# Kernel tuning notes

Measured on AMD Instinct MI355X. Metric: run time of the kernel, lower is better.

## Reference

```python
import jax, jax.numpy as jnp
import numpy as np

ADMP = 16  # admp_channel


def _backbone(x, Wc, bc):
    # Conv2d(3->256, k=3, stride=2, pad=1) + ReLU stands in for feature_backbone
    y = jax.lax.conv_general_dilated(x, Wc, window_strides=(2, 2),
                                     padding=((1, 1), (1, 1)),
                                     dimension_numbers=('NCHW', 'OIHW', 'NCHW'))
    return jax.nn.relu(y + bc[None, :, None, None])


def _feature_select(feat, k):
    # AdaptiveMaxPool2d(k, return_indices=True) on feat.sum(1); H,W divisible by k
    B, C, H, W = feat.shape
    bh, bw = H // k, W // k
    resp = feat.sum(1)  # [B,H,W]
    r = resp.reshape(B, k, bh, k, bw).transpose(0, 1, 3, 2, 4).reshape(B, k, k, bh * bw)
    loc = jnp.argmax(r, axis=-1)            # local flat index in each bh*bw block
    lr, lc = loc // bw, loc % bw
    rows = jnp.arange(k)[None, :, None] * bh + lr   # [B,k,k]
    cols = jnp.arange(k)[None, None, :] * bw + lc
    return (rows * W + cols).reshape(B, k * k)      # flat indices into H*W


def _mlp(x, W1, b1, W2, b2):
    # Linear -> ReLU -> (Dropout eval = identity) -> Linear
    return jax.nn.relu(x @ W1 + b1) @ W2 + b2


def reference(xA, xB, Wconv, bconv, W1r, b1r, W2r, b2r, W1c, b1c, W2c, b2c):
    fA = _backbone(xA, Wconv, bconv)  # [B,C,H,W]
    fB = _backbone(xB, Wconv, bconv)
    B, C, H, W = fA.shape
    N = H * W
    idxA = _feature_select(fA, ADMP)                       # [B,K]
    fA_flat = fA.reshape(B, C, N)
    fB_flat = fB.reshape(B, C, N)
    desc = jnp.take_along_axis(fA_flat, idxA[:, None, :], axis=2)  # [B,C,K]
    # ||a-b||^2 = ||a||^2 - 2 a.b + ||b||^2 ; fused batched kNN
    dist = ((desc ** 2).sum(1)[:, :, None]
            - 2.0 * jnp.einsum('bck,bcn->bkn', desc, fB_flat)
            + (fB_flat ** 2).sum(1)[:, None, :])           # [B,K,N]
    minidx = jnp.argmin(dist, axis=-1)                     # [B,K]
    # original uses high (==width here since H==W) for both div and mod
    row_A, col_A = idxA // H, idxA % H
    row_B, col_B = minidx // H, minidx % H
    drow = (row_B - row_A).astype(jnp.float32)             # [B,K]
    dcol = (col_A - col_B).astype(jnp.float32)
    out_drow = _mlp(drow, W1r, b1r, W2r, b2r)              # [B,1]
    out_dcol = _mlp(dcol, W1c, b1c, W2c, b2c)
    return jnp.concatenate([out_drow, out_dcol], axis=1)   # [B,2]


def setup_inputs() -> dict:
    key = jax.random.key(0)
    ks = jax.random.split(key, 8)
    K2 = ADMP * ADMP
    return {
        'xA': jax.random.normal(ks[0], (4, 3, 256, 256), jnp.float32),
        'xB': jax.random.normal(ks[1], (4, 3, 256, 256), jnp.float32),
        'Wconv': jax.random.normal(ks[2], (256, 3, 3, 3), jnp.float32) * 0.1,
        'bconv': jnp.zeros((256,), jnp.float32),
        'W1r': jax.random.normal(ks[3], (K2, K2 // 2), jnp.float32) * 0.05,
        'b1r': jnp.zeros((K2 // 2,), jnp.float32),
        'W2r': jax.random.normal(ks[4], (K2 // 2, 1), jnp.float32) * 0.05,
        'b2r': jnp.zeros((1,), jnp.float32),
        'W1c': jax.random.normal(ks[5], (K2, K2 // 2), jnp.float32) * 0.05,
        'b1c': jnp.zeros((K2 // 2,), jnp.float32),
        'W2c': jax.random.normal(ks[6], (K2 // 2, 1), jnp.float32) * 0.05,
        'b2c': jnp.zeros((1,), jnp.float32),
    }
```

## Files before the change

### kernel.cpp

```cpp
#include <hip/hip_runtime.h>
#include <stdint.h>

constexpr int NB   = 4;
constexpr int CIN  = 3;
constexpr int HIN  = 256;
constexpr int COUT = 256;
constexpr int HF   = 128;
constexpr int NF   = HF * HF;
constexpr int KADM = 16;
constexpr int KK   = KADM * KADM;
constexpr int HID  = 128;
constexpr int DFB  = 65536;
constexpr int PX   = 32;
constexpr int NT   = NF / PX;

typedef unsigned short ushort_t;
typedef __attribute__((ext_vector_type(8))) _Float16 f16x8;
typedef __attribute__((ext_vector_type(2))) __fp16   fp16v2;
typedef __attribute__((ext_vector_type(4))) float    f32x4;

__device__ inline unsigned long long u64min(unsigned long long a, unsigned long long b) {
    return a < b ? a : b;
}
__device__ inline ushort_t f16bits(_Float16 h) { return __builtin_bit_cast(ushort_t, h); }

__device__ inline int swz(int pix, int c) {
    return pix * 256 + ((((c >> 3) ^ (pix & 7)) << 3) | (c & 7));
}

__device__ inline int dfoff(int w, int chunk, int j, int lane) {
    return (((w * 8 + chunk) * 4 + j) * 64 + lane) * 8;
}

__global__ __launch_bounds__(256) void prep_kernel(
        const float* __restrict__ W, ushort_t* __restrict__ WFh, ushort_t* __restrict__ WFl)
{
    int co = threadIdx.x;
    int w = co >> 6, j = (co >> 4) & 3, la = co & 15;
    #pragma unroll
    for (int q = 0; q < 32; ++q) {
        float v = (q < 27) ? W[co * 27 + q] : 0.f;
        _Float16 h = (_Float16)v;
        _Float16 l = (_Float16)(v - (float)h);
        int lg = q >> 3, e = q & 7;
        int off = ((w * 4 + j) * 64 + lg * 16 + la) * 8 + e;
        WFh[off] = f16bits(h);
        WFl[off] = f16bits(l);
    }
}

__global__ __launch_bounds__(256) void convA_kernel(
        const float* __restrict__ xA,
        const ushort_t* __restrict__ WFh, const ushort_t* __restrict__ WFl,
        const float* __restrict__ bias, float* __restrict__ resp)
{
    __shared__ float    pS[CIN][3][132];
    __shared__ ushort_t Ah[64][40];
    __shared__ ushort_t Al[64][40];
    __shared__ float    redS[4][64];

    int b = blockIdx.y;
    const float* x = xA + (size_t)b * CIN * HIN * HIN;
    int tid = threadIdx.x;
    int lane = tid & 63, w = tid >> 6;
    int la = lane & 15, lg = lane >> 4;
    int wbase = w * 64;

    float bj[4];
    f16x8 bh[4], bl[4];
    #pragma unroll
    for (int j = 0; j < 4; ++j) {
        bj[j] = bias[wbase + j * 16 + la];
        int off = ((w * 4 + j) * 64 + lane) * 8;
        bh[j] = *(const f16x8*)&WFh[off];
        bl[j] = *(const f16x8*)&WFl[off];
    }

    for (int t2 = 0; t2 < 2; ++t2) {
        int tile = blockIdx.x * 2 + t2;
        int oh  = tile >> 1;
        int ow0 = (tile & 1) << 6;

        if (t2) __syncthreads();
        for (int i = tid; i < CIN * 3 * 129; i += 256) {
            int ci = i / (3 * 129);
            int r2 = i % (3 * 129);
            int kh = r2 / 129, c = r2 % 129;
            int gr = 2 * oh - 1 + kh, gc = 2 * ow0 - 1 + c;
            float v = 0.f;
            if (gr >= 0 && gr < HIN && gc >= 0 && gc < HIN)
                v = x[(size_t)ci * HIN * HIN + (size_t)gr * HIN + gc];
            pS[ci][kh][c] = v;
        }
        __syncthreads();

        {
            int n = tid >> 2, qg = tid & 3;
            unsigned uh[4], ul[4];
            #pragma unroll
            for (int e2 = 0; e2 < 4; ++e2) {
                ushort_t hh[2], ll[2];
                #pragma unroll
                for (int s = 0; s < 2; ++s) {
                    int q = qg * 8 + e2 * 2 + s;
                    float v = 0.f;
                    if (q < 27) {
                        int ci = q / 9, r = (q % 9) / 3, kw = q % 3;
                        v = pS[ci][r][2 * n + kw];
                    }
                    _Float16 h = (_Float16)v;
                    _Float16 l = (_Float16)(v - (float)h);
                    hh[s] = f16bits(h); ll[s] = f16bits(l);
                }
                uh[e2] = (unsigned)hh[0] | ((unsigned)hh[1] << 16);
                ul[e2] = (unsigned)ll[0] | ((unsigned)ll[1] << 16);
            }
            *(uint4*)&Ah[n][qg * 8] = *(uint4*)uh;
            *(uint4*)&Al[n][qg * 8] = *(uint4*)ul;
        }
        __syncthreads();

        f16x8 ah[4], al[4];
        #pragma unroll
        for (int i = 0; i < 4; ++i) {
            ah[i] = *(const f16x8*)&Ah[i * 16 + la][lg * 8];
            al[i] = *(const f16x8*)&Al[i * 16 + la][lg * 8];
        }

        f32x4 acc[4][4];
        #pragma unroll
        for (int i = 0; i < 4; ++i)
            #pragma unroll
            for (int j = 0; j < 4; ++j) acc[i][j] = (f32x4)0.f;

        #pragma unroll
        for (int i = 0; i < 4; ++i)
            #pragma unroll
            for (int j = 0; j < 4; ++j) {
                acc[i][j] = __builtin_amdgcn_mfma_f32_16x16x32_f16(ah[i], bh[j], acc[i][j], 0, 0, 0);
                acc[i][j] = __builtin_amdgcn_mfma_f32_16x16x32_f16(al[i], bh[j], acc[i][j], 0, 0, 0);
                acc[i][j] = __builtin_amdgcn_mfma_f32_16x16x32_f16(ah[i], bl[j], acc[i][j], 0, 0, 0);
            }

        float s[4][4];
        #pragma unroll
        for (int i = 0; i < 4; ++i)
            #pragma unroll
            for (int r = 0; r < 4; ++r) s[i][r] = 0.f;

        #pragma unroll
        for (int i = 0; i < 4; ++i)
            #pragma unroll
            for (int j = 0; j < 4; ++j)
                #pragma unroll
                for (int r = 0; r < 4; ++r)
                    s[i][r] += fmaxf(acc[i][j][r] + bj[j], 0.f);

        #pragma unroll
        for (int i = 0; i < 4; ++i)
            #pragma unroll
            for (int r = 0; r < 4; ++r) {
                float v = s[i][r];
                v += __shfl_xor(v, 1, 64);
                v += __shfl_xor(v, 2, 64);
                v += __shfl_xor(v, 4, 64);
                v += __shfl_xor(v, 8, 64);
                s[i][r] = v;
            }
        if (la == 0) {
            #pragma unroll
            for (int i = 0; i < 4; ++i)
                #pragma unroll
                for (int r = 0; r < 4; ++r)
                    redS[w][i * 16 + lg * 4 + r] = s[i][r];
        }
        __syncthreads();
        if (tid < 64) {
            float tot = redS[0][tid] + redS[1][tid] + redS[2][tid] + redS[3][tid];
            resp[(size_t)b * NF + oh * HF + ow0 + tid] = tot;
        }
    }
}

__global__ __launch_bounds__(256) void select_kernel(
        const float* __restrict__ resp,
        const float* __restrict__ xA, const float* __restrict__ W,
        const float* __restrict__ bias,
        int* __restrict__ idxA,
        ushort_t* __restrict__ dFh, ushort_t* __restrict__ dFl,
        float* __restrict__ normA)
{
    __shared__ float patch[27];
    __shared__ float red[4];
    __shared__ int   sidx;

    int bk = blockIdx.x;
    int b = bk >> 8, k = bk & 255;
    int t = threadIdx.x;

    if (t < 64) {
        int kr = k >> 4, kc = k & 15;
        int lr = t >> 3, lc = t & 7;
        int row = kr * 8 + lr, col = kc * 8 + lc;
        float bv = resp[(size_t)b * NF + (size_t)row * HF + col];
        int best = t;
        for (int off = 32; off > 0; off >>= 1) {
            float ov = __shfl_down(bv, off, 64);
            int   oi = __shfl_down(best, off, 64);
            if (ov > bv || (ov == bv && oi < best)) { bv = ov; best = oi; }
        }
        if (t == 0) {
            int r = kr * 8 + (best >> 3), c = kc * 8 + (best & 7);
            int idx = r * HF + c;
            idxA[bk] = idx;
            sidx = idx;
        }
    }
    __syncthreads();
    int idx = sidx;
    int oh = idx >> 7, ow = idx & 127;

    if (t < 27) {
        int ci = t / 9, kh = (t % 9) / 3, kw = t % 3;
        int ir = oh * 2 - 1 + kh, ic = ow * 2 - 1 + kw;
        float v = 0.f;
        if (ir >= 0 && ir < HIN && ic >= 0 && ic < HIN)
            v = xA[((size_t)b * CIN + ci) * HIN * HIN + (size_t)ir * HIN + ic];
        patch[t] = v;
    }
    __syncthreads();

    float v = bias[t];
    const float* w = &W[t * 27];
    #pragma unroll
    for (int q = 0; q < 27; ++q) v = fmaf(patch[q], w[q], v);
    v = fmaxf(v, 0.f);

    _Float16 h = (_Float16)v;
    _Float16 l = (_Float16)(v - (float)h);
    {
        int wq = k >> 6, j = (k >> 4) & 3, la = k & 15;
        int chunk = t >> 5, lg = (t >> 3) & 3, e = t & 7;
        int off = b * DFB + dfoff(wq, chunk, j, lg * 16 + la) + e;
        dFh[off] = f16bits(h);
        dFl[off] = f16bits(l);
    }

    float s = v * v;
    for (int off = 32; off > 0; off >>= 1) s += __shfl_down(s, off, 64);
    if ((t & 63) == 0) red[t >> 6] = s;
    __syncthreads();
    if (t == 0) normA[bk] = red[0] + red[1] + red[2] + red[3];
}

__device__ inline void load_desc(const ushort_t* __restrict__ dFh,
                                 const ushort_t* __restrict__ dFl,
                                 int w, int chunk, int lane,
                                 f16x8* bh, f16x8* bl)
{
    #pragma unroll
    for (int j = 0; j < 4; ++j) {
        int off = dfoff(w, chunk, j, lane);
        bh[j] = *(const f16x8*)&dFh[off];
        bl[j] = *(const f16x8*)&dFl[off];
    }
}

__device__ inline void knn_chunk(const ushort_t* __restrict__ fH,
                                 const ushort_t* __restrict__ fL,
                                 int la, int lg, int cc,
                                 const f16x8* bh, const f16x8* bl,
                                 f32x4 (&acc)[2][4])
{
    #pragma unroll
    for (int i = 0; i < 2; ++i) {
        f16x8 ah = *(const f16x8*)&fH[swz(i * 16 + la, cc + lg * 8)];
        f16x8 al = *(const f16x8*)&fL[swz(i * 16 + la, cc + lg * 8)];
        __builtin_amdgcn_s_setprio(1);
        #pragma unroll
        for (int j = 0; j < 4; ++j) {
            acc[i][j] = __builtin_amdgcn_mfma_f32_16x16x32_f16(ah, bh[j], acc[i][j], 0, 0, 0);
            acc[i][j] = __builtin_amdgcn_mfma_f32_16x16x32_f16(al, bh[j], acc[i][j], 0, 0, 0);
            acc[i][j] = __builtin_amdgcn_mfma_f32_16x16x32_f16(ah, bl[j], acc[i][j], 0, 0, 0);
        }
        __builtin_amdgcn_s_setprio(0);
    }
}

__global__ __launch_bounds__(256, 4) void fused_kernel(
        const float* __restrict__ xB,
        const ushort_t* __restrict__ WFh, const ushort_t* __restrict__ WFl,
        const float* __restrict__ bias,
        const ushort_t* __restrict__ dFhg, const ushort_t* __restrict__ dFlg,
        const float* __restrict__ normA,
        unsigned long long* __restrict__ packed)
{
    __shared__ __align__(16) char smem[2 * PX * 256 * 2];
    __shared__ float redS[4][PX];
    __shared__ float nAS[KK];
    __shared__ float nBS[PX];
    __shared__ float bS[COUT];

    float*    pSp = (float*)smem;
    ushort_t* AhP = (ushort_t*)(smem + 2448);
    ushort_t* AlP = (ushort_t*)(smem + 2448 + 2560);
    ushort_t* fH  = (ushort_t*)smem;
    ushort_t* fL  = (ushort_t*)(smem + PX * 256 * 2);

    int tile = blockIdx.x;
    int b    = blockIdx.y;
    int oh   = tile >> 2;
    int ow0  = (tile & 3) << 5;
    const float* x = xB + (size_t)b * CIN * HIN * HIN;
    int tid = threadIdx.x;

    nAS[tid] = normA[b * KK + tid];
    bS[tid]  = bias[tid];

    for (int i = tid; i < CIN * 3 * 65; i += 256) {
        int ci = i / (3 * 65);
        int r2 = i % (3 * 65);
        int kh = r2 / 65, c = r2 % 65;
        int gr = 2 * oh - 1 + kh, gc = 2 * ow0 - 1 + c;
        float v = 0.f;
        if (gr >= 0 && gr < HIN && gc >= 0 && gc < HIN)
            v = x[(size_t)ci * HIN * HIN + (size_t)gr * HIN + gc];
        pSp[ci * 204 + kh * 68 + c] = v;
    }
    __syncthreads();

    {
        int n = tid >> 3, qg = tid & 7;
        ushort_t hh[4], ll[4];
        #pragma unroll
        for (int s = 0; s < 4; ++s) {
            int q = qg * 4 + s;
            float v = 0.f;
            if (q < 27) {
                int ci = q / 9, r = (q % 9) / 3, kw = q % 3;
                v = pSp[ci * 204 + r * 68 + 2 * n + kw];
            }
            _Float16 h = (_Float16)v;
            _Float16 l = (_Float16)(v - (float)h);
            hh[s] = f16bits(h); ll[s] = f16bits(l);
        }
        unsigned lo, hi;
        lo = (unsigned)hh[0] | ((unsigned)hh[1] << 16);
        hi = (unsigned)hh[2] | ((unsigned)hh[3] << 16);
        *(uint2*)&AhP[n * 40 + qg * 4] = make_uint2(lo, hi);
        lo = (unsigned)ll[0] | ((unsigned)ll[1] << 16);
        hi = (unsigned)ll[2] | ((unsigned)ll[3] << 16);
        *(uint2*)&AlP[n * 40 + qg * 4] = make_uint2(lo, hi);
    }
    __syncthreads();

    int lane = tid & 63, w = tid >> 6;
    int la = lane & 15, lg = lane >> 4;
    int wbase = w * 64;

    f16x8 wah[4], wal[4], pbh[2], pbl[2];
    #pragma unroll
    for (int j = 0; j < 4; ++j) {
        int off = ((w * 4 + j) * 64 + lane) * 8;
        wah[j] = *(const f16x8*)&WFh[off];
        wal[j] = *(const f16x8*)&WFl[off];
    }
    #pragma unroll
    for (int i = 0; i < 2; ++i) {
        pbh[i] = *(const f16x8*)&AhP[(i * 16 + la) * 40 + lg * 8];
        pbl[i] = *(const f16x8*)&AlP[(i * 16 + la) * 40 + lg * 8];
    }

    f32x4 cacc[4][2];
    #pragma unroll
    for (int j = 0; j < 4; ++j)
        #pragma unroll
        for (int i = 0; i < 2; ++i) cacc[j][i] = (f32x4)0.f;

    #pragma unroll
    for (int j = 0; j < 4; ++j)
        #pragma unroll
        for (int i = 0; i < 2; ++i) {
            cacc[j][i] = __builtin_amdgcn_mfma_f32_16x16x32_f16(wah[j], pbh[i], cacc[j][i], 0, 0, 0);
            cacc[j][i] = __builtin_amdgcn_mfma_f32_16x16x32_f16(wal[j], pbh[i], cacc[j][i], 0, 0, 0);
            cacc[j][i] = __builtin_amdgcn_mfma_f32_16x16x32_f16(wah[j], pbl[i], cacc[j][i], 0, 0, 0);
        }

    __syncthreads();

    float s2[2] = {0.f, 0.f};
    #pragma unroll
    for (int j = 0; j < 4; ++j) {
        f32x4 b4 = *(const f32x4*)&bS[wbase + j * 16 + lg * 4];
        int chunk = (wbase + j * 16 + lg * 4) >> 3;
        int within = (lg & 1) * 4;
        #pragma unroll
        for (int i = 0; i < 2; ++i) {
            int pix = i * 16 + la;
            float v0 = fmaxf(cacc[j][i][0] + b4[0], 0.f);
            float v1 = fmaxf(cacc[j][i][1] + b4[1], 0.f);
            float v2 = fmaxf(cacc[j][i][2] + b4[2], 0.f);
            float v3 = fmaxf(cacc[j][i][3] + b4[3], 0.f);
            s2[i] += v0 * v0 + v1 * v1 + v2 * v2 + v3 * v3;
            fp16v2 h01 = __builtin_amdgcn_cvt_pkrtz(v0, v1);
            fp16v2 h23 = __builtin_amdgcn_cvt_pkrtz(v2, v3);
            fp16v2 l01 = __builtin_amdgcn_cvt_pkrtz(v0 - (float)h01[0], v1 - (float)h01[1]);
            fp16v2 l23 = __builtin_amdgcn_cvt_pkrtz(v2 - (float)h23[0], v3 - (float)h23[1]);
            int base = pix * 256 + ((chunk ^ (pix & 7)) << 3) + within;
            *(uint2*)&fH[base] = make_uint2(__builtin_bit_cast(unsigned, h01),
                                            __builtin_bit_cast(unsigned, h23));
            *(uint2*)&fL[base] = make_uint2(__builtin_bit_cast(unsigned, l01),
                                            __builtin_bit_cast(unsigned, l23));
        }
    }

    const ushort_t* dFh = dFhg + (size_t)b * DFB;
    const ushort_t* dFl = dFlg + (size_t)b * DFB;
    f16x8 bhA[4], blA[4], bhB[4], blB[4];
    load_desc(dFh, dFl, w, 0, lane, bhA, blA);
    load_desc(dFh, dFl, w, 1, lane, bhB, blB);

    #pragma unroll
    for (int i = 0; i < 2; ++i) {
        float v = s2[i];
        v += __shfl_xor(v, 16, 64);
        v += __shfl_xor(v, 32, 64);
        if (lg == 0) redS[w][i * 16 + la] = v;
    }
    __syncthreads();
    if (tid < PX) nBS[tid] = redS[0][tid] + redS[1][tid] + redS[2][tid] + redS[3][tid];
    __syncthreads();

    f32x4 acc[2][4];
    #pragma unroll
    for (int i = 0; i < 2; ++i)
        #pragma unroll
        for (int j = 0; j < 4; ++j) acc[i][j] = (f32x4)0.f;

    knn_chunk(fH, fL, la, lg, 0, bhA, blA, acc);
    load_desc(dFh, dFl, w, 2, lane, bhA, blA);
    knn_chunk(fH, fL, la, lg, 32, bhB, blB, acc);
    load_desc(dFh, dFl, w, 3, lane, bhB, blB);
    knn_chunk(fH, fL, la, lg, 64, bhA, blA, acc);
    load_desc(dFh, dFl, w, 4, lane, bhA, blA);
    knn_chunk(fH, fL, la, lg, 96, bhB, blB, acc);
    load_desc(dFh, dFl, w, 5, lane, bhB, blB);
    knn_chunk(fH, fL, la, lg, 128, bhA, blA, acc);
    load_desc(dFh, dFl, w, 6, lane, bhA, blA);
    knn_chunk(fH, fL, la, lg, 160, bhB, blB, acc);
    load_desc(dFh, dFl, w, 7, lane, bhB, blB);
    knn_chunk(fH, fL, la, lg, 192, bhA, blA, acc);
    knn_chunk(fH, fL, la, lg, 224, bhB, blB, acc);

    float nBv[2][4];
    #pragma unroll
    for (int i = 0; i < 2; ++i) {
        f32x4 t4 = *(const f32x4*)&nBS[i * 16 + lg * 4];
        nBv[i][0] = t4[0]; nBv[i][1] = t4[1]; nBv[i][2] = t4[2]; nBv[i][3] = t4[3];
    }
    int n0 = tile * PX;
    float bd[4];
    int   bn[4];
    #pragma unroll
    for (int j = 0; j < 4; ++j) {
        int kl = wbase + j * 16 + la;
        float nAv = nAS[kl];
        float bestd = 3.4e38f;
        int   bestn = 0;
        #pragma unroll
        for (int i = 0; i < 2; ++i)
            #pragma unroll
            for (int r = 0; r < 4; ++r) {
                int n = n0 + i * 16 + lg * 4 + r;
                float d = fmaf(-2.f, acc[i][j][r], nAv) + nBv[i][r];
                if (d < bestd) { bestd = d; bestn = n; }
            }
        #pragma unroll
        for (int off = 16; off <= 32; off <<= 1) {
            float od = __shfl_xor(bestd, off, 64);
            int   on = __shfl_xor(bestn, off, 64);
            bool take = (od < bestd) || (od == bestd && on < bestn);
            bestd = take ? od : bestd;
            bestn = take ? on : bestn;
        }
        bd[j] = bestd; bn[j] = bestn;
    }
    float fd = (lg == 0) ? bd[0] : (lg == 1) ? bd[1] : (lg == 2) ? bd[2] : bd[3];
    int   fn = (lg == 0) ? bn[0] : (lg == 1) ? bn[1] : (lg == 2) ? bn[2] : bn[3];
    unsigned u = __float_as_uint(fd);
    u = (u & 0x80000000u) ? ~u : (u | 0x80000000u);
    unsigned long long key = ((unsigned long long)u << 32) | (unsigned)fn;
    int klw = wbase + lg * 16 + la;
    atomicMin(&packed[b * KK + klw], key);
}

__global__ __launch_bounds__(128) void mlp_kernel(
        const int* __restrict__ idxA, const unsigned long long* __restrict__ packed,
        const float* __restrict__ W1r, const float* __restrict__ b1r,
        const float* __restrict__ W2r, const float* __restrict__ b2r,
        const float* __restrict__ W1c, const float* __restrict__ b1c,
        const float* __restrict__ W2c, const float* __restrict__ b2c,
        float* __restrict__ out)
{
    __shared__ float xS[KK];
    __shared__ float red[2];
    int blk = blockIdx.x;
    int b = blk >> 1, which = blk & 1;
    int t = threadIdx.x;

    for (int k = t; k < KK; k += 128) {
        int ia = idxA[b * KK + k];
        int nn = (int)(packed[b * KK + k] & 0xffffffffULL);
        int rowA = ia >> 7, colA = ia & 127;
        int rowB = nn >> 7, colB = nn & 127;
        xS[k] = (which == 0) ? (float)(rowB - rowA) : (float)(colA - colB);
    }
    __syncthreads();

    const float* W1 = which ? W1c : W1r;
    const float* b1 = which ? b1c : b1r;
    const float* W2 = which ? W2c : W2r;
    const float* b2 = which ? b2c : b2r;

    float h = b1[t];
    for (int k = 0; k < KK; ++k) h = fmaf(xS[k], W1[k * HID + t], h);
    h = fmaxf(h, 0.f);
    float pv = h * W2[t];
    for (int off = 32; off > 0; off >>= 1) pv += __shfl_down(pv, off, 64);
    if ((t & 63) == 0) red[t >> 6] = pv;
    __syncthreads();
    if (t == 0) out[b * 2 + which] = red[0] + red[1] + b2[0];
}

extern "C" void kernel_launch(void* const* d_in, const int* in_sizes, int n_in,
                              void* d_out, int out_size, void* d_ws, size_t ws_size,
                              hipStream_t stream)
{
    const float* xA  = (const float*)d_in[0];
    const float* xB  = (const float*)d_in[1];
    const float* Wc  = (const float*)d_in[2];
    const float* bc  = (const float*)d_in[3];
    const float* W1r = (const float*)d_in[4];
    const float* b1r = (const float*)d_in[5];
    const float* W2r = (const float*)d_in[6];
    const float* b2r = (const float*)d_in[7];
    const float* W1c = (const float*)d_in[8];
    const float* b1c = (const float*)d_in[9];
    const float* W2c = (const float*)d_in[10];
    const float* b2c = (const float*)d_in[11];
    float* out = (float*)d_out;

    char* ws = (char*)d_ws;
    unsigned long long* packed = (unsigned long long*)ws; ws += (size_t)NB * KK * 8;
    int*   idxA   = (int*)ws;      ws += (size_t)NB * KK * 4;
    float* normA  = (float*)ws;    ws += (size_t)NB * KK * 4;
    float* resp   = (float*)ws;    ws += (size_t)NB * NF * 4;
    ushort_t* dFh = (ushort_t*)ws; ws += (size_t)NB * DFB * 2;
    ushort_t* dFl = (ushort_t*)ws; ws += (size_t)NB * DFB * 2;
    ushort_t* WFh = (ushort_t*)ws; ws += (size_t)COUT * 32 * 2;
    ushort_t* WFl = (ushort_t*)ws; ws += (size_t)COUT * 32 * 2;

    hipMemsetAsync(packed, 0xFF, (size_t)NB * KK * 8, stream);

    prep_kernel  <<<1, 256, 0, stream>>>(Wc, WFh, WFl);
    convA_kernel <<<dim3(128, NB), 256, 0, stream>>>(xA, WFh, WFl, bc, resp);
    select_kernel<<<NB * KK, 256, 0, stream>>>(resp, xA, Wc, bc, idxA, dFh, dFl, normA);
    fused_kernel <<<dim3(NT, NB), 256, 0, stream>>>(xB, WFh, WFl, bc, dFh, dFl,
                                                    normA, packed);
    mlp_kernel   <<<8, 128, 0, stream>>>(idxA, packed,
                                         W1r, b1r, W2r, b2r,
                                         W1c, b1c, W2c, b2c, out);
}
```

Before: 72.04 us.

## Double fused kernel pixel tile to 64 with 512 threads; un-loop convA tiles

The fused conv+kNN kernel now processes 64 pixels per block with 8 waves, each wave owning 32 descriptors instead of 64. The weight and descriptor fragment layouts are reorganized per 16-wide k-tile to match, and each lane group handles 4 pixel sub-tiles. This halves the number of blocks and the per-block atomicMin traffic and descriptor reloads, and makes the staged input patch more reusable. convA drops its two-tiles-per-block loop and launches one tile per block instead. In exchange, the larger shared-memory footprint and 512-thread blocks may reduce occupancy.

```diff
diff --git a/kernel.cpp b/kernel.cpp
--- a/kernel.cpp
+++ b/kernel.cpp
@@ -11,7 +11,7 @@
 constexpr int KK   = KADM * KADM;
 constexpr int HID  = 128;
 constexpr int DFB  = 65536;
-constexpr int PX   = 32;
+constexpr int PX   = 64;
 constexpr int NT   = NF / PX;
 
 typedef unsigned short ushort_t;
@@ -19,31 +19,28 @@
 typedef __attribute__((ext_vector_type(2))) __fp16   fp16v2;
 typedef __attribute__((ext_vector_type(4))) float    f32x4;
 
-__device__ inline unsigned long long u64min(unsigned long long a, unsigned long long b) {
-    return a < b ? a : b;
-}
 __device__ inline ushort_t f16bits(_Float16 h) { return __builtin_bit_cast(ushort_t, h); }
 
 __device__ inline int swz(int pix, int c) {
     return pix * 256 + ((((c >> 3) ^ (pix & 7)) << 3) | (c & 7));
 }
 
-__device__ inline int dfoff(int w, int chunk, int j, int lane) {
-    return (((w * 8 + chunk) * 4 + j) * 64 + lane) * 8;
+__device__ inline int dfoff(int kt, int chunk, int lane) {
+    return ((kt * 8 + chunk) * 64 + lane) * 8;
 }
 
 __global__ __launch_bounds__(256) void prep_kernel(
         const float* __restrict__ W, ushort_t* __restrict__ WFh, ushort_t* __restrict__ WFl)
 {
     int co = threadIdx.x;
-    int w = co >> 6, j = (co >> 4) & 3, la = co & 15;
+    int kt = co >> 4, la = co & 15;
     #pragma unroll
     for (int q = 0; q < 32; ++q) {
         float v = (q < 27) ? W[co * 27 + q] : 0.f;
         _Float16 h = (_Float16)v;
         _Float16 l = (_Float16)(v - (float)h);
         int lg = q >> 3, e = q & 7;
-        int off = ((w * 4 + j) * 64 + lg * 16 + la) * 8 + e;
+        int off = (kt * 64 + lg * 16 + la) * 8 + e;
         WFh[off] = f16bits(h);
         WFl[off] = f16bits(l);
     }
@@ -59,9 +56,51 @@
     __shared__ ushort_t Al[64][40];
     __shared__ float    redS[4][64];
 
-    int b = blockIdx.y;
+    int tile = blockIdx.x;
+    int b    = blockIdx.y;
+    int oh   = tile >> 1;
+    int ow0  = (tile & 1) << 6;
     const float* x = xA + (size_t)b * CIN * HIN * HIN;
     int tid = threadIdx.x;
+
+    for (int i = tid; i < CIN * 3 * 129; i += 256) {
+        int ci = i / (3 * 129);
+        int r2 = i % (3 * 129);
+        int kh = r2 / 129, c = r2 % 129;
+        int gr = 2 * oh - 1 + kh, gc = 2 * ow0 - 1 + c;
+        float v = 0.f;
+        if (gr >= 0 && gr < HIN && gc >= 0 && gc < HIN)
+            v = x[(size_t)ci * HIN * HIN + (size_t)gr * HIN + gc];
+        pS[ci][kh][c] = v;
+    }
+    __syncthreads();
+
+    {
+        int n = tid >> 2, qg = tid & 3;
+        unsigned uh[4], ul[4];
+        #pragma unroll
+        for (int e2 = 0; e2 < 4; ++e2) {
+            ushort_t hh[2], ll[2];
+            #pragma unroll
+            for (int s = 0; s < 2; ++s) {
+                int q = qg * 8 + e2 * 2 + s;
+                float v = 0.f;
+                if (q < 27) {
+                    int ci = q / 9, r = (q % 9) / 3, kw = q % 3;
+                    v = pS[ci][r][2 * n + kw];
+                }
+                _Float16 h = (_Float16)v;
+                _Float16 l = (_Float16)(v - (float)h);
+                hh[s] = f16bits(h); ll[s] = f16bits(l);
+            }
+            uh[e2] = (unsigned)hh[0] | ((unsigned)hh[1] << 16);
+            ul[e2] = (unsigned)ll[0] | ((unsigned)ll[1] << 16);
+        }
+        *(uint4*)&Ah[n][qg * 8] = *(uint4*)uh;
+        *(uint4*)&Al[n][qg * 8] = *(uint4*)ul;
+    }
+    __syncthreads();
+
     int lane = tid & 63, w = tid >> 6;
     int la = lane & 15, lg = lane >> 4;
     int wbase = w * 64;
@@ -76,109 +115,64 @@
         bl[j] = *(const f16x8*)&WFl[off];
     }
 
-    for (int t2 = 0; t2 < 2; ++t2) {
-        int tile = blockIdx.x * 2 + t2;
-        int oh  = tile >> 1;
-        int ow0 = (tile & 1) << 6;
-
-        if (t2) __syncthreads();
-        for (int i = tid; i < CIN * 3 * 129; i += 256) {
-            int ci = i / (3 * 129);
-            int r2 = i % (3 * 129);
-            int kh = r2 / 129, c = r2 % 129;
-            int gr = 2 * oh - 1 + kh, gc = 2 * ow0 - 1 + c;
-            float v = 0.f;
-            if (gr >= 0 && gr < HIN && gc >= 0 && gc < HIN)
-                v = x[(size_t)ci * HIN * HIN + (size_t)gr * HIN + gc];
-            pS[ci][kh][c] = v;
-        }
-        __syncthreads();
-
-        {
-            int n = tid >> 2, qg = tid & 3;
-            unsigned uh[4], ul[4];
+    f16x8 ah[4], al[4];
+    #pragma unroll
+    for (int i = 0; i < 4; ++i) {
+        ah[i] = *(const f16x8*)&Ah[i * 16 + la][lg * 8];
+        al[i] = *(const f16x8*)&Al[i * 16 + la][lg * 8];
+    }
+
+    f32x4 acc[4][4];
+    #pragma unroll
+    for (int i = 0; i < 4; ++i)
+        #pragma unroll
+        for (int j = 0; j < 4; ++j) acc[i][j] = (f32x4)0.f;
+
+    #pragma unroll
+    for (int i = 0; i < 4; ++i)
+        #pragma unroll
+        for (int j = 0; j < 4; ++j) {
+            acc[i][j] = __builtin_amdgcn_mfma_f32_16x16x32_f16(ah[i], bh[j], acc[i][j], 0, 0, 0);
+            acc[i][j] = __builtin_amdgcn_mfma_f32_16x16x32_f16(al[i], bh[j], acc[i][j], 0, 0, 0);
+            acc[i][j] = __builtin_amdgcn_mfma_f32_16x16x32_f16(ah[i], bl[j], acc[i][j], 0, 0, 0);
+        }
+
+    float s[4][4];
+    #pragma unroll
+    for (int i = 0; i < 4; ++i)
+        #pragma unroll
+        for (int r = 0; r < 4; ++r) s[i][r] = 0.f;
+
+    #pragma unroll
+    for (int i = 0; i < 4; ++i)
+        #pragma unroll
+        for (int j = 0; j < 4; ++j)
             #pragma unroll
-            for (int e2 = 0; e2 < 4; ++e2) {
-                ushort_t hh[2], ll[2];
-                #pragma unroll
-                for (int s = 0; s < 2; ++s) {
-                    int q = qg * 8 + e2 * 2 + s;
-                    float v = 0.f;
-                    if (q < 27) {
-                        int ci = q / 9, r = (q % 9) / 3, kw = q % 3;
-                        v = pS[ci][r][2 * n + kw];
-                    }
-                    _Float16 h = (_Float16)v;
-                    _Float16 l = (_Float16)(v - (float)h);
-                    hh[s] = f16bits(h); ll[s] = f16bits(l);
-                }
-                uh[e2] = (unsigned)hh[0] | ((unsigned)hh[1] << 16);
-                ul[e2] = (unsigned)ll[0] | ((unsigned)ll[1] << 16);
-            }
-            *(uint4*)&Ah[n][qg * 8] = *(uint4*)uh;
-            *(uint4*)&Al[n][qg * 8] = *(uint4*)ul;
-        }
-        __syncthreads();
-
-        f16x8 ah[4], al[4];
-        #pragma unroll
-        for (int i = 0; i < 4; ++i) {
-            ah[i] = *(const f16x8*)&Ah[i * 16 + la][lg * 8];
-            al[i] = *(const f16x8*)&Al[i * 16 + la][lg * 8];
-        }
-
-        f32x4 acc[4][4];
+            for (int r = 0; r < 4; ++r)
+                s[i][r] += fmaxf(acc[i][j][r] + bj[j], 0.f);
+
+    #pragma unroll
+    for (int i = 0; i < 4; ++i)
+        #pragma unroll
+        for (int r = 0; r < 4; ++r) {
+            float v = s[i][r];
+            v += __shfl_xor(v, 1, 64);
+            v += __shfl_xor(v, 2, 64);
+            v += __shfl_xor(v, 4, 64);
+            v += __shfl_xor(v, 8, 64);
+            s[i][r] = v;
+        }
+    if (la == 0) {
         #pragma unroll
         for (int i = 0; i < 4; ++i)
             #pragma unroll
-            for (int j = 0; j < 4; ++j) acc[i][j] = (f32x4)0.f;
-
-        #pragma unroll
-        for (int i = 0; i < 4; ++i)
-            #pragma unroll
-            for (int j = 0; j < 4; ++j) {
-                acc[i][j] = __builtin_amdgcn_mfma_f32_16x16x32_f16(ah[i], bh[j], acc[i][j], 0, 0, 0);
-                acc[i][j] = __builtin_amdgcn_mfma_f32_16x16x32_f16(al[i], bh[j], acc[i][j], 0, 0, 0);
-                acc[i][j] = __builtin_amdgcn_mfma_f32_16x16x32_f16(ah[i], bl[j], acc[i][j], 0, 0, 0);
-            }
-
-        float s[4][4];
-        #pragma unroll
-        for (int i = 0; i < 4; ++i)
-            #pragma unroll
-            for (int r = 0; r < 4; ++r) s[i][r] = 0.f;
-
-        #pragma unroll
-        for (int i = 0; i < 4; ++i)
-            #pragma unroll
-            for (int j = 0; j < 4; ++j)
-                #pragma unroll
-                for (int r = 0; r < 4; ++r)
-                    s[i][r] += fmaxf(acc[i][j][r] + bj[j], 0.f);
-
-        #pragma unroll
-        for (int i = 0; i < 4; ++i)
-            #pragma unroll
-            for (int r = 0; r < 4; ++r) {
-                float v = s[i][r];
-                v += __shfl_xor(v, 1, 64);
-                v += __shfl_xor(v, 2, 64);
-                v += __shfl_xor(v, 4, 64);
-                v += __shfl_xor(v, 8, 64);
-                s[i][r] = v;
-            }
-        if (la == 0) {
-            #pragma unroll
-            for (int i = 0; i < 4; ++i)
-                #pragma unroll
-                for (int r = 0; r < 4; ++r)
-                    redS[w][i * 16 + lg * 4 + r] = s[i][r];
-        }
-        __syncthreads();
-        if (tid < 64) {
-            float tot = redS[0][tid] + redS[1][tid] + redS[2][tid] + redS[3][tid];
-            resp[(size_t)b * NF + oh * HF + ow0 + tid] = tot;
-        }
+            for (int r = 0; r < 4; ++r)
+                redS[w][i * 16 + lg * 4 + r] = s[i][r];
+    }
+    __syncthreads();
+    if (tid < 64) {
+        float tot = redS[0][tid] + redS[1][tid] + redS[2][tid] + redS[3][tid];
+        resp[(size_t)b * NF + oh * HF + ow0 + tid] = tot;
     }
 }
 
@@ -239,9 +233,9 @@
     _Float16 h = (_Float16)v;
     _Float16 l = (_Float16)(v - (float)h);
     {
-        int wq = k >> 6, j = (k >> 4) & 3, la = k & 15;
+        int kt = k >> 4, la = k & 15;
         int chunk = t >> 5, lg = (t >> 3) & 3, e = t & 7;
-        int off = b * DFB + dfoff(wq, chunk, j, lg * 16 + la) + e;
+        int off = b * DFB + dfoff(kt, chunk, lg * 16 + la) + e;
         dFh[off] = f16bits(h);
         dFl[off] = f16bits(l);
     }
@@ -259,10 +253,10 @@
                                  f16x8* bh, f16x8* bl)
 {
     #pragma unroll
-    for (int j = 0; j < 4; ++j) {
-        int off = dfoff(w, chunk, j, lane);
-        bh[j] = *(const f16x8*)&dFh[off];
-        bl[j] = *(const f16x8*)&dFl[off];
+    for (int jj = 0; jj < 2; ++jj) {
+        int off = dfoff(w * 2 + jj, chunk, lane);
+        bh[jj] = *(const f16x8*)&dFh[off];
+        bl[jj] = *(const f16x8*)&dFl[off];
     }
 }
 
@@ -270,24 +264,24 @@
                                  const ushort_t* __restrict__ fL,
                                  int la, int lg, int cc,
                                  const f16x8* bh, const f16x8* bl,
-                                 f32x4 (&acc)[2][4])
-{
-    #pragma unroll
-    for (int i = 0; i < 2; ++i) {
+                                 f32x4 (&acc)[4][2])
+{
+    #pragma unroll
+    for (int i = 0; i < 4; ++i) {
         f16x8 ah = *(const f16x8*)&fH[swz(i * 16 + la, cc + lg * 8)];
         f16x8 al = *(const f16x8*)&fL[swz(i * 16 + la, cc + lg * 8)];
         __builtin_amdgcn_s_setprio(1);
         #pragma unroll
-        for (int j = 0; j < 4; ++j) {
-            acc[i][j] = __builtin_amdgcn_mfma_f32_16x16x32_f16(ah, bh[j], acc[i][j], 0, 0, 0);
-            acc[i][j] = __builtin_amdgcn_mfma_f32_16x16x32_f16(al, bh[j], acc[i][j], 0, 0, 0);
-            acc[i][j] = __builtin_amdgcn_mfma_f32_16x16x32_f16(ah, bl[j], acc[i][j], 0, 0, 0);
+        for (int jj = 0; jj < 2; ++jj) {
+            acc[i][jj] = __builtin_amdgcn_mfma_f32_16x16x32_f16(ah, bh[jj], acc[i][jj], 0, 0, 0);
+            acc[i][jj] = __builtin_amdgcn_mfma_f32_16x16x32_f16(al, bh[jj], acc[i][jj], 0, 0, 0);
+            acc[i][jj] = __builtin_amdgcn_mfma_f32_16x16x32_f16(ah, bl[jj], acc[i][jj], 0, 0, 0);
         }
         __builtin_amdgcn_s_setprio(0);
     }
 }
 
-__global__ __launch_bounds__(256, 4) void fused_kernel(
+__global__ __launch_bounds__(512, 4) void fused_kernel(
         const float* __restrict__ xB,
         const ushort_t* __restrict__ WFh, const ushort_t* __restrict__ WFl,
         const float* __restrict__ bias,
@@ -296,36 +290,38 @@
         unsigned long long* __restrict__ packed)
 {
     __shared__ __align__(16) char smem[2 * PX * 256 * 2];
-    __shared__ float redS[4][PX];
+    __shared__ float redS[8][PX];
     __shared__ float nAS[KK];
     __shared__ float nBS[PX];
     __shared__ float bS[COUT];
 
     float*    pSp = (float*)smem;
-    ushort_t* AhP = (ushort_t*)(smem + 2448);
-    ushort_t* AlP = (ushort_t*)(smem + 2448 + 2560);
+    ushort_t* AhP = (ushort_t*)(smem + 4752);
+    ushort_t* AlP = (ushort_t*)(smem + 4752 + 5120);
     ushort_t* fH  = (ushort_t*)smem;
     ushort_t* fL  = (ushort_t*)(smem + PX * 256 * 2);
 
     int tile = blockIdx.x;
     int b    = blockIdx.y;
-    int oh   = tile >> 2;
-    int ow0  = (tile & 3) << 5;
+    int oh   = tile >> 1;
+    int ow0  = (tile & 1) << 6;
     const float* x = xB + (size_t)b * CIN * HIN * HIN;
     int tid = threadIdx.x;
 
-    nAS[tid] = normA[b * KK + tid];
-    bS[tid]  = bias[tid];
-
-    for (int i = tid; i < CIN * 3 * 65; i += 256) {
-        int ci = i / (3 * 65);
-        int r2 = i % (3 * 65);
-        int kh = r2 / 65, c = r2 % 65;
+    if (tid < KK) {
+        nAS[tid] = normA[b * KK + tid];
+        bS[tid]  = bias[tid];
+    }
+
+    for (int i = tid; i < CIN * 3 * 129; i += 512) {
+        int ci = i / (3 * 129);
+        int r2 = i % (3 * 129);
+        int kh = r2 / 129, c = r2 % 129;
         int gr = 2 * oh - 1 + kh, gc = 2 * ow0 - 1 + c;
         float v = 0.f;
         if (gr >= 0 && gr < HIN && gc >= 0 && gc < HIN)
             v = x[(size_t)ci * HIN * HIN + (size_t)gr * HIN + gc];
-        pSp[ci * 204 + kh * 68 + c] = v;
+        pSp[ci * 396 + kh * 132 + c] = v;
     }
     __syncthreads();
 
@@ -338,7 +334,7 @@
             float v = 0.f;
             if (q < 27) {
                 int ci = q / 9, r = (q % 9) / 3, kw = q % 3;
-                v = pSp[ci * 204 + r * 68 + 2 * n + kw];
+                v = pSp[ci * 396 + r * 132 + 2 * n + kw];
             }
             _Float16 h = (_Float16)v;
             _Float16 l = (_Float16)(v - (float)h);
@@ -356,51 +352,51 @@
 
     int lane = tid & 63, w = tid >> 6;
     int la = lane & 15, lg = lane >> 4;
-    int wbase = w * 64;
-
-    f16x8 wah[4], wal[4], pbh[2], pbl[2];
-    #pragma unroll
-    for (int j = 0; j < 4; ++j) {
-        int off = ((w * 4 + j) * 64 + lane) * 8;
-        wah[j] = *(const f16x8*)&WFh[off];
-        wal[j] = *(const f16x8*)&WFl[off];
-    }
-    #pragma unroll
-    for (int i = 0; i < 2; ++i) {
+
+    f16x8 wah[2], wal[2], pbh[4], pbl[4];
+    #pragma unroll
+    for (int jj = 0; jj < 2; ++jj) {
+        int off = ((w * 2 + jj) * 64 + lane) * 8;
+        wah[jj] = *(const f16x8*)&WFh[off];
+        wal[jj] = *(const f16x8*)&WFl[off];
+    }
+    #pragma unroll
+    for (int i = 0; i < 4; ++i) {
         pbh[i] = *(const f16x8*)&AhP[(i * 16 + la) * 40 + lg * 8];
         pbl[i] = *(const f16x8*)&AlP[(i * 16 + la) * 40 + lg * 8];
     }
 
-    f32x4 cacc[4][2];
-    #pragma unroll
-    for (int j = 0; j < 4; ++j)
-        #pragma unroll
-        for (int i = 0; i < 2; ++i) cacc[j][i] = (f32x4)0.f;
-
-    #pragma unroll
-    for (int j = 0; j < 4; ++j)
-        #pragma unroll
-        for (int i = 0; i < 2; ++i) {
-            cacc[j][i] = __builtin_amdgcn_mfma_f32_16x16x32_f16(wah[j], pbh[i], cacc[j][i], 0, 0, 0);
-            cacc[j][i] = __builtin_amdgcn_mfma_f32_16x16x32_f16(wal[j], pbh[i], cacc[j][i], 0, 0, 0);
-            cacc[j][i] = __builtin_amdgcn_mfma_f32_16x16x32_f16(wah[j], pbl[i], cacc[j][i], 0, 0, 0);
-        }
-
-    __syncthreads();
-
-    float s2[2] = {0.f, 0.f};
-    #pragma unroll
-    for (int j = 0; j < 4; ++j) {
-        f32x4 b4 = *(const f32x4*)&bS[wbase + j * 16 + lg * 4];
-        int chunk = (wbase + j * 16 + lg * 4) >> 3;
+    f32x4 cacc[2][4];
+    #pragma unroll
+    for (int jj = 0; jj < 2; ++jj)
+        #pragma unroll
+        for (int i = 0; i < 4; ++i) cacc[jj][i] = (f32x4)0.f;
+
+    #pragma unroll
+    for (int jj = 0; jj < 2; ++jj)
+        #pragma unroll
+        for (int i = 0; i < 4; ++i) {
+            cacc[jj][i] = __builtin_amdgcn_mfma_f32_16x16x32_f16(wah[jj], pbh[i], cacc[jj][i], 0, 0, 0);
+            cacc[jj][i] = __builtin_amdgcn_mfma_f32_16x16x32_f16(wal[jj], pbh[i], cacc[jj][i], 0, 0, 0);
+            cacc[jj][i] = __builtin_amdgcn_mfma_f32_16x16x32_f16(wah[jj], pbl[i], cacc[jj][i], 0, 0, 0);
+        }
+
+    __syncthreads();
+
+    float s2[4] = {0.f, 0.f, 0.f, 0.f};
+    #pragma unroll
+    for (int jj = 0; jj < 2; ++jj) {
+        int co4 = (w * 2 + jj) * 16 + lg * 4;
+        f32x4 b4 = *(const f32x4*)&bS[co4];
+        int chunk = co4 >> 3;
         int within = (lg & 1) * 4;
         #pragma unroll
-        for (int i = 0; i < 2; ++i) {
+        for (int i = 0; i < 4; ++i) {
             int pix = i * 16 + la;
-            float v0 = fmaxf(cacc[j][i][0] + b4[0], 0.f);
-            float v1 = fmaxf(cacc[j][i][1] + b4[1], 0.f);
-            float v2 = fmaxf(cacc[j][i][2] + b4[2], 0.f);
-            float v3 = fmaxf(cacc[j][i][3] + b4[3], 0.f);
+            float v0 = fmaxf(cacc[jj][i][0] + b4[0], 0.f);
+            float v1 = fmaxf(cacc[jj][i][1] + b4[1], 0.f);
+            float v2 = fmaxf(cacc[jj][i][2] + b4[2], 0.f);
+            float v3 = fmaxf(cacc[jj][i][3] + b4[3], 0.f);
             s2[i] += v0 * v0 + v1 * v1 + v2 * v2 + v3 * v3;
             fp16v2 h01 = __builtin_amdgcn_cvt_pkrtz(v0, v1);
             fp16v2 h23 = __builtin_amdgcn_cvt_pkrtz(v2, v3);
@@ -416,26 +412,31 @@
 
     const ushort_t* dFh = dFhg + (size_t)b * DFB;
     const ushort_t* dFl = dFlg + (size_t)b * DFB;
-    f16x8 bhA[4], blA[4], bhB[4], blB[4];
+    f16x8 bhA[2], blA[2], bhB[2], blB[2];
     load_desc(dFh, dFl, w, 0, lane, bhA, blA);
     load_desc(dFh, dFl, w, 1, lane, bhB, blB);
 
     #pragma unroll
-    for (int i = 0; i < 2; ++i) {
+    for (int i = 0; i < 4; ++i) {
         float v = s2[i];
         v += __shfl_xor(v, 16, 64);
         v += __shfl_xor(v, 32, 64);
         if (lg == 0) redS[w][i * 16 + la] = v;
     }
     __syncthreads();
-    if (tid < PX) nBS[tid] = redS[0][tid] + redS[1][tid] + redS[2][tid] + redS[3][tid];
-    __syncthreads();
-
-    f32x4 acc[2][4];
-    #pragma unroll
-    for (int i = 0; i < 2; ++i)
-        #pragma unroll
-        for (int j = 0; j < 4; ++j) acc[i][j] = (f32x4)0.f;
+    if (tid < PX) {
+        float t0 = 0.f;
+        #pragma unroll
+        for (int p = 0; p < 8; ++p) t0 += redS[p][tid];
+        nBS[tid] = t0;
+    }
+    __syncthreads();
+
+    f32x4 acc[4][2];
+    #pragma unroll
+    for (int i = 0; i < 4; ++i)
+        #pragma unroll
+        for (int jj = 0; jj < 2; ++jj) acc[i][jj] = (f32x4)0.f;
 
     knn_chunk(fH, fL, la, lg, 0, bhA, blA, acc);
     load_desc(dFh, dFl, w, 2, lane, bhA, blA);
@@ -452,27 +453,27 @@
     knn_chunk(fH, fL, la, lg, 192, bhA, blA, acc);
     knn_chunk(fH, fL, la, lg, 224, bhB, blB, acc);
 
-    float nBv[2][4];
-    #pragma unroll
-    for (int i = 0; i < 2; ++i) {
+    float nBv[4][4];
+    #pragma unroll
+    for (int i = 0; i < 4; ++i) {
         f32x4 t4 = *(const f32x4*)&nBS[i * 16 + lg * 4];
         nBv[i][0] = t4[0]; nBv[i][1] = t4[1]; nBv[i][2] = t4[2]; nBv[i][3] = t4[3];
     }
     int n0 = tile * PX;
-    float bd[4];
-    int   bn[4];
-    #pragma unroll
-    for (int j = 0; j < 4; ++j) {
-        int kl = wbase + j * 16 + la;
+    float bd[2];
+    int   bn[2];
+    #pragma unroll
+    for (int jj = 0; jj < 2; ++jj) {
+        int kl = (w * 2 + jj) * 16 + la;
         float nAv = nAS[kl];
         float bestd = 3.4e38f;
         int   bestn = 0;
         #pragma unroll
-        for (int i = 0; i < 2; ++i)
+        for (int i = 0; i < 4; ++i)
             #pragma unroll
             for (int r = 0; r < 4; ++r) {
                 int n = n0 + i * 16 + lg * 4 + r;
-                float d = fmaf(-2.f, acc[i][j][r], nAv) + nBv[i][r];
+                float d = fmaf(-2.f, acc[i][jj][r], nAv) + nBv[i][r];
                 if (d < bestd) { bestd = d; bestn = n; }
             }
         #pragma unroll
@@ -483,15 +484,17 @@
             bestd = take ? od : bestd;
             bestn = take ? on : bestn;
         }
-        bd[j] = bestd; bn[j] = bestn;
-    }
-    float fd = (lg == 0) ? bd[0] : (lg == 1) ? bd[1] : (lg == 2) ? bd[2] : bd[3];
-    int   fn = (lg == 0) ? bn[0] : (lg == 1) ? bn[1] : (lg == 2) ? bn[2] : bn[3];
-    unsigned u = __float_as_uint(fd);
-    u = (u & 0x80000000u) ? ~u : (u | 0x80000000u);
-    unsigned long long key = ((unsigned long long)u << 32) | (unsigned)fn;
-    int klw = wbase + lg * 16 + la;
-    atomicMin(&packed[b * KK + klw], key);
+        bd[jj] = bestd; bn[jj] = bestn;
+    }
+    if (lg < 2) {
+        float fd = (lg == 0) ? bd[0] : bd[1];
+        int   fn = (lg == 0) ? bn[0] : bn[1];
+        unsigned u = __float_as_uint(fd);
+        u = (u & 0x80000000u) ? ~u : (u | 0x80000000u);
+        unsigned long long key = ((unsigned long long)u << 32) | (unsigned)fn;
+        int klw = (w * 2 + lg) * 16 + la;
+        atomicMin(&packed[b * KK + klw], key);
+    }
 }
 
 __global__ __launch_bounds__(128) void mlp_kernel(
@@ -563,9 +566,9 @@
     hipMemsetAsync(packed, 0xFF, (size_t)NB * KK * 8, stream);
 
     prep_kernel  <<<1, 256, 0, stream>>>(Wc, WFh, WFl);
-    convA_kernel <<<dim3(128, NB), 256, 0, stream>>>(xA, WFh, WFl, bc, resp);
+    convA_kernel <<<dim3(256, NB), 256, 0, stream>>>(xA, WFh, WFl, bc, resp);
     select_kernel<<<NB * KK, 256, 0, stream>>>(resp, xA, Wc, bc, idxA, dFh, dFl, normA);
-    fused_kernel <<<dim3(NT, NB), 256, 0, stream>>>(xB, WFh, WFl, bc, dFh, dFl,
+    fused_kernel <<<dim3(NT, NB), 512, 0, stream>>>(xB, WFh, WFl, bc, dFh, dFl,
                                                     normA, packed);
     mlp_kernel   <<<8, 128, 0, stream>>>(idxA, packed,
                                          W1r, b1r, W2r, b2r,
```

Measured after the change: 60.26 us. 1.2x faster.
